# Optimization experiments

Measured on AMD Instinct MI355X. Metric: run time of the kernel, lower is better.

## Reference

```python
import jax, jax.numpy as jnp
import numpy as np

N_TOKENS = 16384
MODEL_DIM = 2048
NUM_EXPERTS = 64
K = 2


def setup_inputs() -> dict:
    key = jax.random.key(0)
    k1, k2 = jax.random.split(key)
    inputs = jax.random.normal(k1, (N_TOKENS, MODEL_DIM), dtype=jnp.float32)
    # gate weight, torch Linear(model_dim, num_experts, bias=False) -> [E, D]
    wg_weight = jax.random.normal(k2, (NUM_EXPERTS, MODEL_DIM), dtype=jnp.float32) * 0.02
    return {"inputs": inputs, "wg_weight": wg_weight}


def reference(inputs, wg_weight):
    E = wg_weight.shape[0]
    # gate computed in fp32 (module casts input and keeps wg in float32)
    logits = jnp.einsum("nd,ed->ne", inputs.astype(jnp.float32), wg_weight)
    probs = jax.nn.softmax(logits, axis=-1)                      # [N, E]
    topk_probs, topk_indices = jax.lax.top_k(probs, K)           # [N, K]
    flat_idx = topk_indices.reshape(-1)                          # [N*K]
    # stable sort of expert ids over all (token, slot) pairs
    sort_ordering = jnp.argsort(flat_idx)                        # [N*K]
    # reverse permutation: reversed[sort_ordering[i]] = i
    ar = jnp.arange(flat_idx.shape[0], dtype=sort_ordering.dtype)
    reversed_ordering = jnp.zeros_like(sort_ordering).at[sort_ordering].set(ar)
    # map slot index back to token index
    token_order = sort_ordering // K
    # per-expert counts (== unique_consecutive counts scattered into [E])
    input_splits = jnp.bincount(flat_idx, length=E).astype(jnp.int64)
    # combine weights: renormalize top-k probs via softmax when k > 1
    if K > 1:
        combine_weights = jax.nn.softmax(topk_probs, axis=-1)
    else:
        combine_weights = topk_probs
    combine_weights = combine_weights.reshape(-1).astype(inputs.dtype)
    return token_order, reversed_ordering, combine_weights, input_splits, probs
```

## Files before the change

kernel.cpp:

```cpp
#include <hip/hip_runtime.h>
#include <math.h>

#define N_TOKENS    16384
#define MODEL_DIM   2048
#define NUM_EXPERTS 64
#define NK          (N_TOKENS * 2)

#define OFF_TOKEN_ORDER 0
#define OFF_REVERSED    (NK)
#define OFF_COMBINE     (2 * NK)
#define OFF_SPLITS      (3 * NK)
#define OFF_PROBS       (3 * NK + NUM_EXPERTS)

#define BT 64
#define BK 64
#define NSEG 256
#define LSTRIDE 65

__global__ __launch_bounds__(256) void gate_partial(
    const float* __restrict__ x,
    const float* __restrict__ w,
    float* __restrict__ partials,
    int S, int kslice)
{
    __shared__ float a_tile[BT * 64];
    __shared__ float b_tile[NUM_EXPERTS * BK];

    const int tid = threadIdx.x;
    const int tb = blockIdx.x;
    const int sp = blockIdx.y;
    const int t0 = tb * BT;
    const int kbase = sp * kslice;
    const int tx = tid & 15;
    const int ty = tid >> 4;
    const int lk = tid & 15;
    const int lrow = tid >> 4;

    double accd[4][4];
#pragma unroll
    for (int i = 0; i < 4; i++)
#pragma unroll
        for (int j = 0; j < 4; j++) accd[i][j] = 0.0;

    for (int k0 = kbase; k0 < kbase + kslice; k0 += BK) {
#pragma unroll
        for (int j = 0; j < 4; j++) {
            const int row = lrow + j * 16;
            const int sc = ((lk + (row >> 2)) & 15) * 4;
            const float4 va = *(const float4*)(x + (size_t)(t0 + row) * MODEL_DIM + k0 + lk * 4);
            *(float4*)(a_tile + row * 64 + sc) = va;
            const float4 vb = *(const float4*)(w + (size_t)row * MODEL_DIM + k0 + lk * 4);
            *(float4*)(b_tile + row * 64 + sc) = vb;
        }
        __syncthreads();

        float accf[4][4];
#pragma unroll
        for (int i = 0; i < 4; i++)
#pragma unroll
            for (int j = 0; j < 4; j++) accf[i][j] = 0.0f;

#pragma unroll 4
        for (int k4 = 0; k4 < 16; k4++) {
            const int ca = ((k4 + ty) & 15) * 4;
            const int cb = ((k4 + tx) & 15) * 4;
            float4 a[4], b[4];
#pragma unroll
            for (int i = 0; i < 4; i++) a[i] = *(const float4*)(a_tile + (ty * 4 + i) * 64 + ca);
#pragma unroll
            for (int j = 0; j < 4; j++) b[j] = *(const float4*)(b_tile + (tx * 4 + j) * 64 + cb);
#pragma unroll
            for (int i = 0; i < 4; i++)
#pragma unroll
                for (int j = 0; j < 4; j++) {
                    accf[i][j] += a[i].x * b[j].x;
                    accf[i][j] += a[i].y * b[j].y;
                    accf[i][j] += a[i].z * b[j].z;
                    accf[i][j] += a[i].w * b[j].w;
                }
        }
#pragma unroll
        for (int i = 0; i < 4; i++)
#pragma unroll
            for (int j = 0; j < 4; j++) accd[i][j] += (double)accf[i][j];
        __syncthreads();
    }

    float* dst = partials + ((size_t)tb * S + sp) * 4096;
#pragma unroll
    for (int i = 0; i < 4; i++) {
        float4 v;
        v.x = (float)accd[i][0]; v.y = (float)accd[i][1];
        v.z = (float)accd[i][2]; v.w = (float)accd[i][3];
        *(float4*)(dst + (ty * 4 + i) * 64 + tx * 4) = v;
    }
}

__global__ __launch_bounds__(256) void reduce_kernel(
    const float* __restrict__ partials,
    float* __restrict__ out,
    int* __restrict__ flat_idx,
    int* __restrict__ segHist,
    int S)
{
    __shared__ float l_lds[BT * LSTRIDE];
    __shared__ float inv_lds[BT];
    __shared__ int hist[NUM_EXPERTS];

    const int tid = threadIdx.x;
    const int tb = blockIdx.x;
    const int t0 = tb * BT;
    const float* src = partials + (size_t)tb * S * 4096;

#pragma unroll
    for (int v = 0; v < 4; v++) {
        const int q = tid + v * 256;
        double a0 = 0.0, a1 = 0.0, a2 = 0.0, a3 = 0.0;
        for (int s = 0; s < S; s++) {
            const float4 p = *(const float4*)(src + (size_t)s * 4096 + q * 4);
            a0 += (double)p.x; a1 += (double)p.y; a2 += (double)p.z; a3 += (double)p.w;
        }
        const int f = q * 4;
        const int t = f >> 6;
        const int e = f & 63;
        float* row = l_lds + t * LSTRIDE + e;
        row[0] = (float)a0; row[1] = (float)a1; row[2] = (float)a2; row[3] = (float)a3;
    }
    if (tid < NUM_EXPERTS) hist[tid] = 0;
    __syncthreads();

    if (tid < BT) {
        const int t = tid;
        float* row = l_lds + t * LSTRIDE;
        float m = -INFINITY;
#pragma unroll
        for (int e = 0; e < NUM_EXPERTS; e++) m = fmaxf(m, row[e]);
        float l1 = -INFINITY, l2 = -INFINITY;
        int i1 = 0, i2 = 0;
        double s = 0.0;
        for (int e = 0; e < NUM_EXPERTS; e++) {
            const float l = row[e];
            if (l > l1) { l2 = l1; i2 = i1; l1 = l; i1 = e; }
            else if (l > l2) { l2 = l; i2 = e; }
            const float ex = expf(l - m);
            s += (double)ex;
            row[e] = ex;
        }
        const float inv = (float)(1.0 / s);
        inv_lds[t] = inv;
        const float p1 = expf(l1 - m) * inv;
        const float p2 = expf(l2 - m) * inv;
        const float e2 = expf(p2 - p1);
        const float r = 1.0f / (1.0f + e2);
        const int gtok = t0 + t;
        out[OFF_COMBINE + 2 * gtok]     = r;
        out[OFF_COMBINE + 2 * gtok + 1] = e2 * r;
        flat_idx[2 * gtok]     = i1;
        flat_idx[2 * gtok + 1] = i2;
        atomicAdd(&hist[i1], 1);
        atomicAdd(&hist[i2], 1);
    }
    __syncthreads();

    if (tid < NUM_EXPERTS) segHist[tb * NUM_EXPERTS + tid] = hist[tid];

#pragma unroll
    for (int r4 = 0; r4 < 4; r4++) {
        const int f = r4 * 1024 + tid * 4;
        const int t = f >> 6;
        const int e = f & 63;
        const float inv = inv_lds[t];
        float4 v;
        v.x = l_lds[t * LSTRIDE + e + 0] * inv;
        v.y = l_lds[t * LSTRIDE + e + 1] * inv;
        v.z = l_lds[t * LSTRIDE + e + 2] * inv;
        v.w = l_lds[t * LSTRIDE + e + 3] * inv;
        *(float4*)(out + OFF_PROBS + (size_t)(t0 + t) * NUM_EXPERTS + e) = v;
    }
}

__global__ __launch_bounds__(256) void scan_kernel(
    const int* __restrict__ segHist, int* __restrict__ segOff,
    float* __restrict__ out)
{
    __shared__ int h[NSEG * NUM_EXPERTS];
    __shared__ int gtot[4 * NUM_EXPERTS];
    __shared__ int base[NUM_EXPERTS];
    const int tid = threadIdx.x;
    for (int i = tid; i < NSEG * NUM_EXPERTS / 4; i += 256)
        *(int4*)(h + i * 4) = *(const int4*)(segHist + i * 4);
    __syncthreads();

    const int e = tid & 63;
    const int g = tid >> 6;
    int run = 0;
    for (int s = g * 64; s < g * 64 + 64; s++) {
        const int idx = s * NUM_EXPERTS + e;
        const int v = h[idx];
        h[idx] = run;
        run += v;
    }
    gtot[g * NUM_EXPERTS + e] = run;
    __syncthreads();

    if (tid < NUM_EXPERTS) {
        int b = 0;
#pragma unroll
        for (int gg = 0; gg < 4; gg++) {
            const int t = gtot[gg * NUM_EXPERTS + tid];
            gtot[gg * NUM_EXPERTS + tid] = b;
            b += t;
        }
        out[OFF_SPLITS + tid] = (float)b;
        int xs = b;
#pragma unroll
        for (int off = 1; off < 64; off <<= 1) {
            const int v = __shfl_up(xs, off);
            if (tid >= off) xs += v;
        }
        base[tid] = xs - b;
    }
    __syncthreads();

    const int myoff = gtot[g * NUM_EXPERTS + e] + base[e];
    for (int s = g * 64; s < g * 64 + 64; s++) {
        const int idx = s * NUM_EXPERTS + e;
        segOff[idx] = h[idx] + myoff;
    }
}

__global__ __launch_bounds__(256) void scatter_kernel(
    const int* __restrict__ flat_idx, const int* __restrict__ segOff,
    float* __restrict__ out)
{
    __shared__ int cnt[2 * NUM_EXPERTS];
    const int tid = threadIdx.x;
    const int i = blockIdx.x * 256 + tid;
    const int e = flat_idx[i];
    const int lane = tid & 63;
    const int wv = tid >> 6;
    const int segslot = wv >> 1;
    const int seg = i >> 7;

    if (tid < 2 * NUM_EXPERTS) cnt[tid] = 0;
    __syncthreads();

    unsigned long long match = ~0ull;
#pragma unroll
    for (int b = 0; b < 6; b++) {
        const unsigned long long m = __ballot((e >> b) & 1);
        match &= ((e >> b) & 1) ? m : ~m;
    }
    const int rank = __popcll(match & ((1ull << lane) - 1ull));

    int pos = 0;
    if ((wv & 1) == 0) {
        pos = segOff[seg * NUM_EXPERTS + e] + rank;
        if (lane == __builtin_ctzll(match))
            cnt[segslot * NUM_EXPERTS + e] = __popcll(match);
    }
    __syncthreads();
    if ((wv & 1) == 1)
        pos = segOff[seg * NUM_EXPERTS + e] + cnt[segslot * NUM_EXPERTS + e] + rank;

    out[OFF_TOKEN_ORDER + pos] = (float)(i >> 1);
    out[OFF_REVERSED + i]      = (float)pos;
}

extern "C" void kernel_launch(void* const* d_in, const int* in_sizes, int n_in,
                              void* d_out, int out_size, void* d_ws, size_t ws_size,
                              hipStream_t stream) {
    const float* x = (const float*)d_in[0];
    const float* w = (const float*)d_in[1];
    float* out = (float*)d_out;

    int* flat_idx = (int*)d_ws;
    int* segHist  = flat_idx + NK;
    int* segOff   = segHist + NSEG * NUM_EXPERTS;
    float* ws_part = (float*)(segOff + NSEG * NUM_EXPERTS);

    const size_t fixed_bytes = ((size_t)NK + 2 * NSEG * NUM_EXPERTS) * 4;
    const size_t avail = ws_size > fixed_bytes ? ws_size - fixed_bytes : 0;
    const size_t part1 = (size_t)N_TOKENS * NUM_EXPERTS * 4;

    int S;
    float* partials = ws_part;
    if      (avail >= 8 * part1) S = 8;
    else if (avail >= 4 * part1) S = 4;
    else if (avail >= 2 * part1) S = 2;
    else if (avail >= 1 * part1) S = 1;
    else { S = 1; partials = out + OFF_PROBS; }
    const int kslice = MODEL_DIM / S;

    gate_partial<<<dim3(N_TOKENS / BT, S), 256, 0, stream>>>(x, w, partials, S, kslice);
    reduce_kernel<<<NSEG, 256, 0, stream>>>(partials, out, flat_idx, segHist, S);
    scan_kernel<<<1, 256, 0, stream>>>(segHist, segOff, out);
    scatter_kernel<<<NK / 256, 256, 0, stream>>>(flat_idx, segOff, out);
}
```

Measured before the change: 249.0 us.

## Fuse reduce, scan and scatter into one kernel; retile GEMM with direct LDS loads

The gate GEMM now uses 128-token tiles with BK=32, a fixed 8-way K split and global_load_lds direct-to-LDS copies. It keeps the fp32 partial sums in float rather than double and sets launch bounds to allow more waves per SIMD. The reduce, scan and scatter kernels are merged into one kernel: the last block to arrive, detected by an atomic counter, computes the expert prefix sums while the other blocks spin-wait on a flag. This removes two kernel launches and the flat_idx round trip through global memory. The spin-wait assumes all 256 blocks are co-resident, and the fixed split drops the old workspace-size fallback.

```diff
diff --git a/kernel.cpp b/kernel.cpp
--- a/kernel.cpp
+++ b/kernel.cpp
@@ -12,124 +12,153 @@
 #define OFF_SPLITS      (3 * NK)
 #define OFF_PROBS       (3 * NK + NUM_EXPERTS)
 
-#define BT 64
-#define BK 64
+#define BT 128
+#define BK 32
+#define S_SPLITS 8
 #define NSEG 256
 #define LSTRIDE 65
 
-__global__ __launch_bounds__(256) void gate_partial(
+typedef const __attribute__((address_space(1))) void g_void;
+typedef __attribute__((address_space(3))) void l_void;
+
+__global__ __launch_bounds__(256, 3) void gate_partial(
     const float* __restrict__ x,
     const float* __restrict__ w,
     float* __restrict__ partials,
-    int S, int kslice)
+    int* __restrict__ ctrl)
 {
-    __shared__ float a_tile[BT * 64];
-    __shared__ float b_tile[NUM_EXPERTS * BK];
+    __shared__ __align__(16) float a_tile[BT * BK];
+    __shared__ __align__(16) float b_tile[NUM_EXPERTS * BK];
 
     const int tid = threadIdx.x;
     const int tb = blockIdx.x;
     const int sp = blockIdx.y;
+    if (tb == 0 && sp == 0 && tid == 0) { ctrl[0] = 0; ctrl[1] = 0; }
+
     const int t0 = tb * BT;
-    const int kbase = sp * kslice;
+    const int kbase = sp * (MODEL_DIM / S_SPLITS);
+    const int wv = tid >> 6, ln = tid & 63;
     const int tx = tid & 15;
     const int ty = tid >> 4;
-    const int lk = tid & 15;
-    const int lrow = tid >> 4;
-
-    double accd[4][4];
-#pragma unroll
-    for (int i = 0; i < 4; i++)
-#pragma unroll
-        for (int j = 0; j < 4; j++) accd[i][j] = 0.0;
-
-    for (int k0 = kbase; k0 < kbase + kslice; k0 += BK) {
-#pragma unroll
-        for (int j = 0; j < 4; j++) {
-            const int row = lrow + j * 16;
-            const int sc = ((lk + (row >> 2)) & 15) * 4;
-            const float4 va = *(const float4*)(x + (size_t)(t0 + row) * MODEL_DIM + k0 + lk * 4);
-            *(float4*)(a_tile + row * 64 + sc) = va;
-            const float4 vb = *(const float4*)(w + (size_t)row * MODEL_DIM + k0 + lk * 4);
-            *(float4*)(b_tile + row * 64 + sc) = vb;
-        }
-        __syncthreads();
-
-        float accf[4][4];
-#pragma unroll
-        for (int i = 0; i < 4; i++)
+
+    int a_row[4], a_ch[4], b_row[2], b_ch[2];
+#pragma unroll
+    for (int q = 0; q < 4; q++) {
+        const int p = wv * 4096 + q * 1024 + ln * 16;
+        const int row = p >> 7;
+        const int cp = (p >> 4) & 7;
+        a_row[q] = row;
+        a_ch[q] = (cp - (row >> 3)) & 7;
+    }
+#pragma unroll
+    for (int q = 0; q < 2; q++) {
+        const int p = wv * 2048 + q * 1024 + ln * 16;
+        const int row = p >> 7;
+        const int cp = (p >> 4) & 7;
+        b_row[q] = row;
+        b_ch[q] = (cp - (row >> 3)) & 7;
+    }
+
+    float fold[8][4];
+#pragma unroll
+    for (int i = 0; i < 8; i++)
+#pragma unroll
+        for (int j = 0; j < 4; j++) fold[i][j] = 0.0f;
+
+    for (int tile = 0; tile < 8; tile++) {
+        const int k0 = kbase + tile * BK;
+#pragma unroll
+        for (int q = 0; q < 4; q++)
+            __builtin_amdgcn_global_load_lds(
+                (g_void*)(x + (size_t)(t0 + a_row[q]) * MODEL_DIM + k0 + a_ch[q] * 4),
+                (l_void*)((char*)a_tile + wv * 4096 + q * 1024), 16, 0, 0);
+#pragma unroll
+        for (int q = 0; q < 2; q++)
+            __builtin_amdgcn_global_load_lds(
+                (g_void*)(w + (size_t)b_row[q] * MODEL_DIM + k0 + b_ch[q] * 4),
+                (l_void*)((char*)b_tile + wv * 2048 + q * 1024), 16, 0, 0);
+        __syncthreads();
+
+        float accf[8][4];
+#pragma unroll
+        for (int i = 0; i < 8; i++)
 #pragma unroll
             for (int j = 0; j < 4; j++) accf[i][j] = 0.0f;
 
-#pragma unroll 4
-        for (int k4 = 0; k4 < 16; k4++) {
-            const int ca = ((k4 + ty) & 15) * 4;
-            const int cb = ((k4 + tx) & 15) * 4;
-            float4 a[4], b[4];
-#pragma unroll
-            for (int i = 0; i < 4; i++) a[i] = *(const float4*)(a_tile + (ty * 4 + i) * 64 + ca);
-#pragma unroll
-            for (int j = 0; j < 4; j++) b[j] = *(const float4*)(b_tile + (tx * 4 + j) * 64 + cb);
-#pragma unroll
-            for (int i = 0; i < 4; i++)
-#pragma unroll
-                for (int j = 0; j < 4; j++) {
-                    accf[i][j] += a[i].x * b[j].x;
-                    accf[i][j] += a[i].y * b[j].y;
-                    accf[i][j] += a[i].z * b[j].z;
-                    accf[i][j] += a[i].w * b[j].w;
-                }
-        }
-#pragma unroll
-        for (int i = 0; i < 4; i++)
-#pragma unroll
-            for (int j = 0; j < 4; j++) accd[i][j] += (double)accf[i][j];
-        __syncthreads();
-    }
-
-    float* dst = partials + ((size_t)tb * S + sp) * 4096;
-#pragma unroll
-    for (int i = 0; i < 4; i++) {
+#pragma unroll
+        for (int k4 = 0; k4 < 8; k4++) {
+            const float* ap = a_tile + ty * 256 + ((k4 + ty) & 7) * 4;
+            const float* bp = b_tile + tx * 128 + ((k4 + (tx >> 1)) & 7) * 4;
+            const float4 b0 = *(const float4*)(bp);
+            const float4 b1 = *(const float4*)(bp + 32);
+            const float4 b2 = *(const float4*)(bp + 64);
+            const float4 b3 = *(const float4*)(bp + 96);
+#pragma unroll
+            for (int i = 0; i < 8; i++) {
+                const float4 a = *(const float4*)(ap + i * 32);
+                accf[i][0] += a.x * b0.x + a.y * b0.y + a.z * b0.z + a.w * b0.w;
+                accf[i][1] += a.x * b1.x + a.y * b1.y + a.z * b1.z + a.w * b1.w;
+                accf[i][2] += a.x * b2.x + a.y * b2.y + a.z * b2.z + a.w * b2.w;
+                accf[i][3] += a.x * b3.x + a.y * b3.y + a.z * b3.z + a.w * b3.w;
+            }
+        }
+#pragma unroll
+        for (int i = 0; i < 8; i++)
+#pragma unroll
+            for (int j = 0; j < 4; j++) fold[i][j] += accf[i][j];
+        __syncthreads();
+    }
+
+    float* dst = partials + ((size_t)tb * S_SPLITS + sp) * (BT * 64);
+#pragma unroll
+    for (int i = 0; i < 8; i++) {
         float4 v;
-        v.x = (float)accd[i][0]; v.y = (float)accd[i][1];
-        v.z = (float)accd[i][2]; v.w = (float)accd[i][3];
-        *(float4*)(dst + (ty * 4 + i) * 64 + tx * 4) = v;
+        v.x = fold[i][0]; v.y = fold[i][1]; v.z = fold[i][2]; v.w = fold[i][3];
+        *(float4*)(dst + (ty * 8 + i) * 64 + tx * 4) = v;
     }
 }
 
-__global__ __launch_bounds__(256) void reduce_kernel(
+__global__ __launch_bounds__(256) void moe_post(
     const float* __restrict__ partials,
     float* __restrict__ out,
-    int* __restrict__ flat_idx,
     int* __restrict__ segHist,
-    int S)
+    int* __restrict__ segOff,
+    int* __restrict__ ctrl)
 {
-    __shared__ float l_lds[BT * LSTRIDE];
-    __shared__ float inv_lds[BT];
+    __shared__ int h[NSEG * NUM_EXPERTS];
+    __shared__ float inv_lds[64];
     __shared__ int hist[NUM_EXPERTS];
-
+    __shared__ int flat_e[128];
+    __shared__ int cnt[NUM_EXPERTS];
+    __shared__ int segOffL[NUM_EXPERTS];
+    __shared__ int gtot[4 * NUM_EXPERTS];
+    __shared__ int base[NUM_EXPERTS];
+    __shared__ int islast;
+
+    float* l_lds = (float*)h;
     const int tid = threadIdx.x;
     const int tb = blockIdx.x;
-    const int t0 = tb * BT;
-    const float* src = partials + (size_t)tb * S * 4096;
+    const int t0 = tb * 64;
+    const int pb = tb >> 1, half = tb & 1;
 
 #pragma unroll
     for (int v = 0; v < 4; v++) {
         const int q = tid + v * 256;
+        const int t = q >> 4;
+        const int c = (q & 15) * 4;
         double a0 = 0.0, a1 = 0.0, a2 = 0.0, a3 = 0.0;
-        for (int s = 0; s < S; s++) {
-            const float4 p = *(const float4*)(src + (size_t)s * 4096 + q * 4);
+        for (int s = 0; s < S_SPLITS; s++) {
+            const float4 p = *(const float4*)(partials +
+                ((size_t)(pb * S_SPLITS + s)) * (BT * 64) + (half * 64 + t) * 64 + c);
             a0 += (double)p.x; a1 += (double)p.y; a2 += (double)p.z; a3 += (double)p.w;
         }
-        const int f = q * 4;
-        const int t = f >> 6;
-        const int e = f & 63;
-        float* row = l_lds + t * LSTRIDE + e;
+        float* row = l_lds + t * LSTRIDE + c;
         row[0] = (float)a0; row[1] = (float)a1; row[2] = (float)a2; row[3] = (float)a3;
     }
     if (tid < NUM_EXPERTS) hist[tid] = 0;
     __syncthreads();
 
-    if (tid < BT) {
+    if (tid < 64) {
         const int t = tid;
         float* row = l_lds + t * LSTRIDE;
         float m = -INFINITY;
@@ -155,14 +184,16 @@
         const int gtok = t0 + t;
         out[OFF_COMBINE + 2 * gtok]     = r;
         out[OFF_COMBINE + 2 * gtok + 1] = e2 * r;
-        flat_idx[2 * gtok]     = i1;
-        flat_idx[2 * gtok + 1] = i2;
+        flat_e[2 * t]     = i1;
+        flat_e[2 * t + 1] = i2;
         atomicAdd(&hist[i1], 1);
         atomicAdd(&hist[i2], 1);
     }
     __syncthreads();
 
-    if (tid < NUM_EXPERTS) segHist[tb * NUM_EXPERTS + tid] = hist[tid];
+    if (tid < NUM_EXPERTS)
+        __hip_atomic_store(&segHist[tb * NUM_EXPERTS + tid], hist[tid],
+                           __ATOMIC_RELAXED, __HIP_MEMORY_SCOPE_AGENT);
 
 #pragma unroll
     for (int r4 = 0; r4 < 4; r4++) {
@@ -177,94 +208,96 @@
         v.w = l_lds[t * LSTRIDE + e + 3] * inv;
         *(float4*)(out + OFF_PROBS + (size_t)(t0 + t) * NUM_EXPERTS + e) = v;
     }
-}
-
-__global__ __launch_bounds__(256) void scan_kernel(
-    const int* __restrict__ segHist, int* __restrict__ segOff,
-    float* __restrict__ out)
-{
-    __shared__ int h[NSEG * NUM_EXPERTS];
-    __shared__ int gtot[4 * NUM_EXPERTS];
-    __shared__ int base[NUM_EXPERTS];
-    const int tid = threadIdx.x;
-    for (int i = tid; i < NSEG * NUM_EXPERTS / 4; i += 256)
-        *(int4*)(h + i * 4) = *(const int4*)(segHist + i * 4);
-    __syncthreads();
-
-    const int e = tid & 63;
-    const int g = tid >> 6;
-    int run = 0;
-    for (int s = g * 64; s < g * 64 + 64; s++) {
-        const int idx = s * NUM_EXPERTS + e;
-        const int v = h[idx];
-        h[idx] = run;
-        run += v;
-    }
-    gtot[g * NUM_EXPERTS + e] = run;
-    __syncthreads();
+    __syncthreads();
+
+    if (tid == 0) {
+        const int old = __hip_atomic_fetch_add(&ctrl[0], 1,
+                            __ATOMIC_ACQ_REL, __HIP_MEMORY_SCOPE_AGENT);
+        islast = (old == NSEG - 1);
+    }
+    __syncthreads();
+
+    if (islast) {
+        for (int i = tid; i < NSEG * NUM_EXPERTS; i += 256)
+            h[i] = __hip_atomic_load(&segHist[i], __ATOMIC_RELAXED, __HIP_MEMORY_SCOPE_AGENT);
+        __syncthreads();
+        const int e = tid & 63;
+        const int g = tid >> 6;
+        int run = 0;
+        for (int s = g * 64; s < g * 64 + 64; s++) {
+            const int idx = s * NUM_EXPERTS + e;
+            const int v = h[idx];
+            h[idx] = run;
+            run += v;
+        }
+        gtot[g * NUM_EXPERTS + e] = run;
+        __syncthreads();
+        if (tid < NUM_EXPERTS) {
+            int b = 0;
+#pragma unroll
+            for (int gg = 0; gg < 4; gg++) {
+                const int t = gtot[gg * NUM_EXPERTS + tid];
+                gtot[gg * NUM_EXPERTS + tid] = b;
+                b += t;
+            }
+            out[OFF_SPLITS + tid] = (float)b;
+            int xs = b;
+#pragma unroll
+            for (int off = 1; off < 64; off <<= 1) {
+                const int v = __shfl_up(xs, off);
+                if (tid >= off) xs += v;
+            }
+            base[tid] = xs - b;
+        }
+        __syncthreads();
+        const int myoff = gtot[g * NUM_EXPERTS + e] + base[e];
+        for (int s = g * 64; s < g * 64 + 64; s++) {
+            const int idx = s * NUM_EXPERTS + e;
+            __hip_atomic_store(&segOff[idx], h[idx] + myoff,
+                               __ATOMIC_RELAXED, __HIP_MEMORY_SCOPE_AGENT);
+        }
+        __syncthreads();
+        if (tid == 0)
+            __hip_atomic_store(&ctrl[1], 1, __ATOMIC_RELEASE, __HIP_MEMORY_SCOPE_AGENT);
+    } else {
+        if (tid == 0)
+            while (__hip_atomic_load(&ctrl[1], __ATOMIC_ACQUIRE, __HIP_MEMORY_SCOPE_AGENT) == 0)
+                __builtin_amdgcn_s_sleep(2);
+        __syncthreads();
+    }
 
     if (tid < NUM_EXPERTS) {
-        int b = 0;
-#pragma unroll
-        for (int gg = 0; gg < 4; gg++) {
-            const int t = gtot[gg * NUM_EXPERTS + tid];
-            gtot[gg * NUM_EXPERTS + tid] = b;
-            b += t;
-        }
-        out[OFF_SPLITS + tid] = (float)b;
-        int xs = b;
-#pragma unroll
-        for (int off = 1; off < 64; off <<= 1) {
-            const int v = __shfl_up(xs, off);
-            if (tid >= off) xs += v;
-        }
-        base[tid] = xs - b;
-    }
-    __syncthreads();
-
-    const int myoff = gtot[g * NUM_EXPERTS + e] + base[e];
-    for (int s = g * 64; s < g * 64 + 64; s++) {
-        const int idx = s * NUM_EXPERTS + e;
-        segOff[idx] = h[idx] + myoff;
-    }
-}
-
-__global__ __launch_bounds__(256) void scatter_kernel(
-    const int* __restrict__ flat_idx, const int* __restrict__ segOff,
-    float* __restrict__ out)
-{
-    __shared__ int cnt[2 * NUM_EXPERTS];
-    const int tid = threadIdx.x;
-    const int i = blockIdx.x * 256 + tid;
-    const int e = flat_idx[i];
+        segOffL[tid] = __hip_atomic_load(&segOff[tb * NUM_EXPERTS + tid],
+                                         __ATOMIC_RELAXED, __HIP_MEMORY_SCOPE_AGENT);
+        cnt[tid] = 0;
+    }
+    __syncthreads();
+
+    int e = 0, rank = 0, pos = 0;
+    unsigned long long match = 0;
     const int lane = tid & 63;
-    const int wv = tid >> 6;
-    const int segslot = wv >> 1;
-    const int seg = i >> 7;
-
-    if (tid < 2 * NUM_EXPERTS) cnt[tid] = 0;
-    __syncthreads();
-
-    unsigned long long match = ~0ull;
-#pragma unroll
-    for (int b = 0; b < 6; b++) {
-        const unsigned long long m = __ballot((e >> b) & 1);
-        match &= ((e >> b) & 1) ? m : ~m;
-    }
-    const int rank = __popcll(match & ((1ull << lane) - 1ull));
-
-    int pos = 0;
-    if ((wv & 1) == 0) {
-        pos = segOff[seg * NUM_EXPERTS + e] + rank;
-        if (lane == __builtin_ctzll(match))
-            cnt[segslot * NUM_EXPERTS + e] = __popcll(match);
-    }
-    __syncthreads();
-    if ((wv & 1) == 1)
-        pos = segOff[seg * NUM_EXPERTS + e] + cnt[segslot * NUM_EXPERTS + e] + rank;
-
-    out[OFF_TOKEN_ORDER + pos] = (float)(i >> 1);
-    out[OFF_REVERSED + i]      = (float)pos;
+    const int wvv = tid >> 6;
+    if (tid < 128) {
+        e = flat_e[tid];
+        match = ~0ull;
+#pragma unroll
+        for (int b = 0; b < 6; b++) {
+            const unsigned long long m = __ballot((e >> b) & 1);
+            match &= ((e >> b) & 1) ? m : ~m;
+        }
+        rank = __popcll(match & ((1ull << lane) - 1ull));
+        if (wvv == 0) {
+            pos = segOffL[e] + rank;
+            if (lane == __builtin_ctzll(match)) cnt[e] = __popcll(match);
+        }
+    }
+    __syncthreads();
+    if (tid < 128) {
+        if (wvv == 1) pos = segOffL[e] + cnt[e] + rank;
+        const int ig = tb * 128 + tid;
+        out[OFF_TOKEN_ORDER + pos] = (float)(ig >> 1);
+        out[OFF_REVERSED + ig]     = (float)pos;
+    }
 }
 
 extern "C" void kernel_launch(void* const* d_in, const int* in_sizes, int n_in,
@@ -274,26 +307,12 @@
     const float* w = (const float*)d_in[1];
     float* out = (float*)d_out;
 
-    int* flat_idx = (int*)d_ws;
-    int* segHist  = flat_idx + NK;
-    int* segOff   = segHist + NSEG * NUM_EXPERTS;
-    float* ws_part = (float*)(segOff + NSEG * NUM_EXPERTS);
-
-    const size_t fixed_bytes = ((size_t)NK + 2 * NSEG * NUM_EXPERTS) * 4;
-    const size_t avail = ws_size > fixed_bytes ? ws_size - fixed_bytes : 0;
-    const size_t part1 = (size_t)N_TOKENS * NUM_EXPERTS * 4;
-
-    int S;
-    float* partials = ws_part;
-    if      (avail >= 8 * part1) S = 8;
-    else if (avail >= 4 * part1) S = 4;
-    else if (avail >= 2 * part1) S = 2;
-    else if (avail >= 1 * part1) S = 1;
-    else { S = 1; partials = out + OFF_PROBS; }
-    const int kslice = MODEL_DIM / S;
-
-    gate_partial<<<dim3(N_TOKENS / BT, S), 256, 0, stream>>>(x, w, partials, S, kslice);
-    reduce_kernel<<<NSEG, 256, 0, stream>>>(partials, out, flat_idx, segHist, S);
-    scan_kernel<<<1, 256, 0, stream>>>(segHist, segOff, out);
-    scatter_kernel<<<NK / 256, 256, 0, stream>>>(flat_idx, segOff, out);
+    int* ctrl    = (int*)d_ws;
+    int* segHist = ctrl + 4;
+    int* segOff  = segHist + NSEG * NUM_EXPERTS;
+    float* partials = (float*)(segOff + NSEG * NUM_EXPERTS);
+
+    gate_partial<<<dim3(BT == 128 ? N_TOKENS / BT : 0, S_SPLITS), 256, 0, stream>>>(
+        x, w, partials, ctrl);
+    moe_post<<<NSEG, 256, 0, stream>>>(partials, out, segHist, segOff, ctrl);
 }
```

Result: slower. 896.6 us (+260.0%).

## Restructure gate GEMM: one token per lane, wave-uniform weight loads, drop fp64 accumulation

Applied to the files above, without the earlier changes.

Each lane now owns one token row and each wave handles 16 experts. Weights are read through wave-uniform (readfirstlane) addresses directly from global memory, so the shared-memory weight tile is gone. The per-tile fp64 accumulation is replaced with plain fp32 accumulators. This cuts LDS traffic and the double-precision adds, but the per-thread register tile shrinks, so compute intensity per LDS load drops and the kernel relies on scalar/broadcast loads of the weights hitting in cache. Dropping fp64 accumulation may also change numerical results relative to the reference top-k ordering.

```diff
diff --git a/kernel.cpp b/kernel.cpp
--- a/kernel.cpp
+++ b/kernel.cpp
@@ -23,76 +23,52 @@
     float* __restrict__ partials,
     int S, int kslice)
 {
-    __shared__ float a_tile[BT * 64];
-    __shared__ float b_tile[NUM_EXPERTS * BK];
+    __shared__ __align__(16) float a_tile[BT * BK];
 
     const int tid = threadIdx.x;
     const int tb = blockIdx.x;
     const int sp = blockIdx.y;
     const int t0 = tb * BT;
     const int kbase = sp * kslice;
-    const int tx = tid & 15;
-    const int ty = tid >> 4;
-    const int lk = tid & 15;
-    const int lrow = tid >> 4;
-
-    double accd[4][4];
-#pragma unroll
-    for (int i = 0; i < 4; i++)
-#pragma unroll
-        for (int j = 0; j < 4; j++) accd[i][j] = 0.0;
+    const int lane = tid & 63;
+    const int e0 = __builtin_amdgcn_readfirstlane((tid >> 6) << 4);
+
+    const int srow = tid >> 4;
+    const int sc = tid & 15;
+
+    float acc[16];
+#pragma unroll
+    for (int j = 0; j < 16; j++) acc[j] = 0.0f;
 
     for (int k0 = kbase; k0 < kbase + kslice; k0 += BK) {
 #pragma unroll
-        for (int j = 0; j < 4; j++) {
-            const int row = lrow + j * 16;
-            const int sc = ((lk + (row >> 2)) & 15) * 4;
-            const float4 va = *(const float4*)(x + (size_t)(t0 + row) * MODEL_DIM + k0 + lk * 4);
-            *(float4*)(a_tile + row * 64 + sc) = va;
-            const float4 vb = *(const float4*)(w + (size_t)row * MODEL_DIM + k0 + lk * 4);
-            *(float4*)(b_tile + row * 64 + sc) = vb;
+        for (int g = 0; g < 4; g++) {
+            const int row = g * 16 + srow;
+            const float4 v = *(const float4*)(x + (size_t)(t0 + row) * MODEL_DIM + k0 + sc * 4);
+            const int phys = (sc + row) & 15;
+            *(float4*)(a_tile + row * 64 + phys * 4) = v;
         }
         __syncthreads();
 
-        float accf[4][4];
-#pragma unroll
-        for (int i = 0; i < 4; i++)
-#pragma unroll
-            for (int j = 0; j < 4; j++) accf[i][j] = 0.0f;
-
-#pragma unroll 4
+#pragma unroll
         for (int k4 = 0; k4 < 16; k4++) {
-            const int ca = ((k4 + ty) & 15) * 4;
-            const int cb = ((k4 + tx) & 15) * 4;
-            float4 a[4], b[4];
-#pragma unroll
-            for (int i = 0; i < 4; i++) a[i] = *(const float4*)(a_tile + (ty * 4 + i) * 64 + ca);
-#pragma unroll
-            for (int j = 0; j < 4; j++) b[j] = *(const float4*)(b_tile + (tx * 4 + j) * 64 + cb);
-#pragma unroll
-            for (int i = 0; i < 4; i++)
-#pragma unroll
-                for (int j = 0; j < 4; j++) {
-                    accf[i][j] += a[i].x * b[j].x;
-                    accf[i][j] += a[i].y * b[j].y;
-                    accf[i][j] += a[i].z * b[j].z;
-                    accf[i][j] += a[i].w * b[j].w;
-                }
-        }
-#pragma unroll
-        for (int i = 0; i < 4; i++)
-#pragma unroll
-            for (int j = 0; j < 4; j++) accd[i][j] += (double)accf[i][j];
+            const float4 a = *(const float4*)(a_tile + lane * 64 + ((k4 + lane) & 15) * 4);
+#pragma unroll
+            for (int j = 0; j < 16; j++) {
+                const float4 b = *(const float4*)(w + (size_t)(e0 + j) * MODEL_DIM + k0 + k4 * 4);
+                acc[j] += a.x * b.x + a.y * b.y + a.z * b.z + a.w * b.w;
+            }
+        }
         __syncthreads();
     }
 
-    float* dst = partials + ((size_t)tb * S + sp) * 4096;
-#pragma unroll
-    for (int i = 0; i < 4; i++) {
+    float* dst = partials + ((size_t)(tb * S + sp) * BT) * 64 + lane * 64 + e0;
+#pragma unroll
+    for (int j4 = 0; j4 < 4; j4++) {
         float4 v;
-        v.x = (float)accd[i][0]; v.y = (float)accd[i][1];
-        v.z = (float)accd[i][2]; v.w = (float)accd[i][3];
-        *(float4*)(dst + (ty * 4 + i) * 64 + tx * 4) = v;
+        v.x = acc[j4 * 4 + 0]; v.y = acc[j4 * 4 + 1];
+        v.z = acc[j4 * 4 + 2]; v.w = acc[j4 * 4 + 3];
+        *(float4*)(dst + j4 * 4) = v;
     }
 }
 
```

New measurement: 595.4 us. 2.39x slower.
